# Kernel optimization log

Hardware: AMD Instinct MI355X
Metric: run time of the kernel (lower is better)

Reference implementation:

```python
import jax, jax.numpy as jnp
import numpy as np

B, H, S, DK = 2, 16, 2048, 64


def setup_inputs() -> dict:
    key = jax.random.key(0)
    kq, kk, kv = jax.random.split(key, 3)
    q = jax.random.normal(kq, (B, H, S, DK), dtype=jnp.float32)
    k = jax.random.normal(kk, (B, H, S, DK), dtype=jnp.float32)
    v = jax.random.normal(kv, (B, H, S, DK), dtype=jnp.float32)
    # 3-D boolean mask [B, Sq, Sk]; True = allowed. Causal lower-triangular.
    mask = jnp.broadcast_to(jnp.tril(jnp.ones((S, S), dtype=bool)), (B, S, S))
    return {"q": q, "k": k, "v": v, "mask": mask}


def reference(q, k, v, mask):
    # scores: [B, H, Sq, Sk]
    scores = jnp.einsum("bhqd,bhkd->bhqk", q, k) / jnp.sqrt(jnp.asarray(DK, q.dtype))
    if mask.ndim == scores.ndim - 1:
        mask = mask[:, None, :, :]  # broadcast over heads
    scores = jnp.where(mask, scores, jnp.asarray(-jnp.inf, scores.dtype))
    attn = jax.nn.softmax(scores, axis=-1)
    out = jnp.einsum("bhqk,bhkd->bhqd", attn, v)
    return out
```

## Files before the change

kernel.cpp:

```cpp
#include <hip/hip_runtime.h>


typedef float    v4f __attribute__((ext_vector_type(4)));
typedef _Float16 v4h __attribute__((ext_vector_type(4)));
typedef _Float16 v8h __attribute__((ext_vector_type(8)));

#define SEQ 2048
#define DKC 64

#if __has_builtin(__builtin_amdgcn_exp2f)
#define EXP2(x) __builtin_amdgcn_exp2f(x)
#else
#define EXP2(x) exp2f(x)
#endif

#define MFMA16(a,b,c) __builtin_amdgcn_mfma_f32_16x16x32_f16(a,b,c,0,0,0)
#undef MFMA16
#define MFMA16(a,b,c) __builtin_amdgcn_mfma_f32_16x16x16f16(a,b,c,0,0,0)
#define MFMA32(a,b,c) __builtin_amdgcn_mfma_f32_16x16x32_f16(a,b,c,0,0,0)

__global__ __launch_bounds__(256) void prep_k(const float* __restrict__ k,
                                              _Float16* __restrict__ kh) {
  const int bh = blockIdx.x;
  const int kt = blockIdx.y;
  const int tid  = threadIdx.x;
  const int quad = tid & 3;
  const int l16  = (tid >> 2) & 15;
  const int st   = (tid >> 6) & 1;
  const int s    = tid >> 7;
  const int krow = kt * 32 + s * 16 + l16;
  const int d    = st * 32 + quad * 8;
  const float* src = k + ((size_t)bh * SEQ + krow) * DKC + d;
  float4 a = *(const float4*)src;
  float4 b = *(const float4*)(src + 4);
  v8h h;
  h[0] = (_Float16)a.x; h[1] = (_Float16)a.y; h[2] = (_Float16)a.z; h[3] = (_Float16)a.w;
  h[4] = (_Float16)b.x; h[5] = (_Float16)b.y; h[6] = (_Float16)b.z; h[7] = (_Float16)b.w;
  _Float16* dst = kh + (size_t)bh * SEQ * DKC
                     + (size_t)(kt * 4 + s * 2 + st) * 512 + l16 * 32 + quad * 8;
  *(v8h*)dst = h;
}

__global__ __launch_bounds__(256) void tr_v(const float* __restrict__ v,
                                            _Float16* __restrict__ vt) {
  const int bh = blockIdx.x, kc = blockIdx.y;
  const int d  = threadIdx.x & 63, kq = threadIdx.x >> 6;
  const float* src = v + ((size_t)bh * SEQ + kc * 64) * DKC;
  _Float16* dstb = vt + (size_t)bh * SEQ * DKC + (size_t)kc * 64 * DKC;
#pragma unroll
  for (int kbl = 0; kbl < 4; ++kbl) {
    const int kl0 = kbl * 16 + kq * 4;
    float x0 = src[(size_t)(kl0 + 0) * DKC + d];
    float x1 = src[(size_t)(kl0 + 1) * DKC + d];
    float x2 = src[(size_t)(kl0 + 2) * DKC + d];
    float x3 = src[(size_t)(kl0 + 3) * DKC + d];
    v4h h;
    h[0] = (_Float16)x0; h[1] = (_Float16)x1; h[2] = (_Float16)x2; h[3] = (_Float16)x3;
    *(v4h*)(dstb + ((size_t)(kbl * 64 + d)) * 16 + kq * 4) = h;
  }
}

__device__ __forceinline__ void load_chunk(const _Float16* __restrict__ khb,
                                           const _Float16* __restrict__ vtb,
                                           int kt, int kOff, int vOff,
                                           v8h (&kf)[4], v4h (&va)[8]) {
  const _Float16* kp = khb + (size_t)kt * 2048;
  const _Float16* vp = vtb + (size_t)kt * 2048;
#pragma unroll
  for (int i = 0; i < 4; ++i) kf[i] = *(const v8h*)(kp + i * 512 + kOff);
#pragma unroll
  for (int i = 0; i < 8; ++i) va[i] = *(const v4h*)(vp + i * 256 + vOff);
}

__device__ __forceinline__ void compute_chunk(int kt, int wkt, int qw, int l16, int quad,
                                              const v8h (&qf)[2][2],
                                              const v8h (&kf)[4], const v4h (&va)[8],
                                              v4f (&O)[2][4], v4f (&L)[2],
                                              const v4h ones) {
  v4f S[2][2] = {};
#pragma unroll
  for (int t = 0; t < 2; ++t)
#pragma unroll
    for (int s = 0; s < 2; ++s) {
      S[t][s] = MFMA32(kf[s * 2 + 0], qf[t][0], S[t][s]);
      S[t][s] = MFMA32(kf[s * 2 + 1], qf[t][1], S[t][s]);
    }

  if (kt == wkt - 1) {
    const int k0 = kt * 32;
#pragma unroll
    for (int t = 0; t < 2; ++t) {
      const int qg = qw + t * 16 + l16;
#pragma unroll
      for (int s = 0; s < 2; ++s) {
        const int kb = k0 + s * 16 + quad * 4;
#pragma unroll
        for (int r = 0; r < 4; ++r)
          if (kb + r > qg) S[t][s][r] = -3e38f;
      }
    }
  }

  v4h pf[2][2];
#pragma unroll
  for (int t = 0; t < 2; ++t)
#pragma unroll
    for (int s = 0; s < 2; ++s) {
      v4h p;
#pragma unroll
      for (int r = 0; r < 4; ++r) p[r] = (_Float16)EXP2(S[t][s][r]);
      pf[t][s] = p;
    }

#pragma unroll
  for (int dc = 0; dc < 4; ++dc) {
    O[0][dc] = MFMA16(va[0 * 4 + dc], pf[0][0], O[0][dc]);
    O[0][dc] = MFMA16(va[1 * 4 + dc], pf[0][1], O[0][dc]);
    O[1][dc] = MFMA16(va[0 * 4 + dc], pf[1][0], O[1][dc]);
    O[1][dc] = MFMA16(va[1 * 4 + dc], pf[1][1], O[1][dc]);
  }
  L[0] = MFMA16(ones, pf[0][0], L[0]);
  L[0] = MFMA16(ones, pf[0][1], L[0]);
  L[1] = MFMA16(ones, pf[1][0], L[1]);
  L[1] = MFMA16(ones, pf[1][1], L[1]);
}

__global__ __launch_bounds__(128, 2) void fa_fwd(const float* __restrict__ q,
                                                 const _Float16* __restrict__ kh,
                                                 const _Float16* __restrict__ vt,
                                                 float* __restrict__ out) {
  const int lane = threadIdx.x & 63;
  const int wid  = threadIdx.x >> 6;
  const int quad = lane >> 4;
  const int l16  = lane & 15;

  const int bh = blockIdx.x & 31;
  const int pr = (int)blockIdx.x >> 5;
  const int qp = wid ? (63 - pr) : pr;
  const int qw = qp * 32;
  const size_t base = (size_t)bh * SEQ * DKC;
  const _Float16* khb = kh + base;
  const _Float16* vtb = vt + base;

  const float CSC = 0.18033688011112042f;
  v8h qf[2][2];
#pragma unroll
  for (int t = 0; t < 2; ++t)
#pragma unroll
    for (int st = 0; st < 2; ++st) {
      const float* qr = q + base + (size_t)(qw + t * 16 + l16) * DKC + st * 32 + quad * 8;
      float4 a = *(const float4*)qr;
      float4 b = *(const float4*)(qr + 4);
      v8h h;
      h[0] = (_Float16)(a.x * CSC); h[1] = (_Float16)(a.y * CSC);
      h[2] = (_Float16)(a.z * CSC); h[3] = (_Float16)(a.w * CSC);
      h[4] = (_Float16)(b.x * CSC); h[5] = (_Float16)(b.y * CSC);
      h[6] = (_Float16)(b.z * CSC); h[7] = (_Float16)(b.w * CSC);
      qf[t][st] = h;
    }

  v4f O[2][4] = {};
  v4f L[2]    = {};
  const v4h ones = {(_Float16)1.f, (_Float16)1.f, (_Float16)1.f, (_Float16)1.f};

  const int wkt = qp + 1;
  const int kOff = l16 * 32 + quad * 8;
  const int vOff = l16 * 16 + quad * 4;

  v8h kfA[4], kfB[4];
  v4h vaA[8], vaB[8];

  load_chunk(khb, vtb, 0, kOff, vOff, kfA, vaA);

  int kt = 0;
  while (true) {
    if (kt + 1 < wkt) load_chunk(khb, vtb, kt + 1, kOff, vOff, kfB, vaB);
    compute_chunk(kt, wkt, qw, l16, quad, qf, kfA, vaA, O, L, ones);
    if (++kt >= wkt) break;

    if (kt + 1 < wkt) load_chunk(khb, vtb, kt + 1, kOff, vOff, kfA, vaA);
    compute_chunk(kt, wkt, qw, l16, quad, qf, kfB, vaB, O, L, ones);
    if (++kt >= wkt) break;
  }

#pragma unroll
  for (int t = 0; t < 2; ++t) {
    const float inv = 1.0f / L[t][0];
    float* orow = out + base + (size_t)(qw + t * 16 + l16) * DKC + quad * 4;
#pragma unroll
    for (int dc = 0; dc < 4; ++dc) {
      float4 w;
      w.x = O[t][dc][0] * inv; w.y = O[t][dc][1] * inv;
      w.z = O[t][dc][2] * inv; w.w = O[t][dc][3] * inv;
      *(float4*)(orow + dc * 16) = w;
    }
  }
}

extern "C" void kernel_launch(void* const* d_in, const int* in_sizes, int n_in,
                              void* d_out, int out_size, void* d_ws, size_t ws_size,
                              hipStream_t stream) {
  (void)in_sizes; (void)n_in; (void)out_size; (void)ws_size;
  const float* q = (const float*)d_in[0];
  const float* k = (const float*)d_in[1];
  const float* v = (const float*)d_in[2];
  float* out = (float*)d_out;

  _Float16* kh = (_Float16*)d_ws;
  _Float16* vt = (_Float16*)((char*)d_ws + (size_t)32 * SEQ * DKC * 2);

  prep_k<<<dim3(32, 64), dim3(256), 0, stream>>>(k, kh);
  tr_v<<<dim3(32, 32), dim3(256), 0, stream>>>(v, vt);
  fa_fwd<<<dim3(1024), dim3(128), 0, stream>>>(q, kh, vt, out);
}
```

Before: 146.8 us.

## Split each query tile's key range across two waves and merge via LDS

Previously each wave in a block handled one of two paired query tiles (short and long causal rows) over the full key range. Now both waves process the same query tile together, each covering half of its key chunks, and then handle the paired tile. Partial O and L accumulators are merged through shared memory before the output is written. The V transpose layout also changes so each lane loads 8-half vectors instead of 4-half ones, with fewer loads per chunk. This evens out per-wave work and shortens the critical path, at the cost of two block barriers and LDS traffic per tile.

```diff
diff --git a/kernel.cpp b/kernel.cpp
--- a/kernel.cpp
+++ b/kernel.cpp
@@ -14,8 +14,6 @@
 #define EXP2(x) exp2f(x)
 #endif
 
-#define MFMA16(a,b,c) __builtin_amdgcn_mfma_f32_16x16x32_f16(a,b,c,0,0,0)
-#undef MFMA16
 #define MFMA16(a,b,c) __builtin_amdgcn_mfma_f32_16x16x16f16(a,b,c,0,0,0)
 #define MFMA32(a,b,c) __builtin_amdgcn_mfma_f32_16x16x32_f16(a,b,c,0,0,0)
 
@@ -43,40 +41,34 @@
 
 __global__ __launch_bounds__(256) void tr_v(const float* __restrict__ v,
                                             _Float16* __restrict__ vt) {
-  const int bh = blockIdx.x, kc = blockIdx.y;
-  const int d  = threadIdx.x & 63, kq = threadIdx.x >> 6;
-  const float* src = v + ((size_t)bh * SEQ + kc * 64) * DKC;
-  _Float16* dstb = vt + (size_t)bh * SEQ * DKC + (size_t)kc * 64 * DKC;
-#pragma unroll
-  for (int kbl = 0; kbl < 4; ++kbl) {
-    const int kl0 = kbl * 16 + kq * 4;
-    float x0 = src[(size_t)(kl0 + 0) * DKC + d];
-    float x1 = src[(size_t)(kl0 + 1) * DKC + d];
-    float x2 = src[(size_t)(kl0 + 2) * DKC + d];
-    float x3 = src[(size_t)(kl0 + 3) * DKC + d];
-    v4h h;
-    h[0] = (_Float16)x0; h[1] = (_Float16)x1; h[2] = (_Float16)x2; h[3] = (_Float16)x3;
-    *(v4h*)(dstb + ((size_t)(kbl * 64 + d)) * 16 + kq * 4) = h;
-  }
-}
-
-__device__ __forceinline__ void load_chunk(const _Float16* __restrict__ khb,
-                                           const _Float16* __restrict__ vtb,
-                                           int kt, int kOff, int vOff,
-                                           v8h (&kf)[4], v4h (&va)[8]) {
-  const _Float16* kp = khb + (size_t)kt * 2048;
-  const _Float16* vp = vtb + (size_t)kt * 2048;
-#pragma unroll
-  for (int i = 0; i < 4; ++i) kf[i] = *(const v8h*)(kp + i * 512 + kOff);
-#pragma unroll
-  for (int i = 0; i < 8; ++i) va[i] = *(const v4h*)(vp + i * 256 + vOff);
+  const int bh = blockIdx.x, kt = blockIdx.y;
+  const int d = threadIdx.x & 63, quad = threadIdx.x >> 6;
+  const float* src = v + ((size_t)bh * SEQ + kt * 32) * DKC + d;
+  v8h h;
+#pragma unroll
+  for (int j = 0; j < 4; ++j) h[j]     = (_Float16)src[(size_t)(quad * 4 + j) * DKC];
+#pragma unroll
+  for (int j = 0; j < 4; ++j) h[4 + j] = (_Float16)src[(size_t)(16 + quad * 4 + j) * DKC];
+  _Float16* dst = vt + (size_t)bh * SEQ * DKC + (size_t)kt * 2048
+                     + (d >> 4) * 512 + (quad * 16 + (d & 15)) * 8;
+  *(v8h*)dst = h;
+}
+
+__device__ __forceinline__ void load_chunk(const _Float16* __restrict__ khl,
+                                           const _Float16* __restrict__ vtl,
+                                           int kt, v8h (&kf)[4], v8h (&va)[4]) {
+  const _Float16* kp = khl + (size_t)kt * 2048;
+  const _Float16* vp = vtl + (size_t)kt * 2048;
+#pragma unroll
+  for (int i = 0; i < 4; ++i) kf[i] = *(const v8h*)(kp + i * 512);
+#pragma unroll
+  for (int i = 0; i < 4; ++i) va[i] = *(const v8h*)(vp + i * 512);
 }
 
 __device__ __forceinline__ void compute_chunk(int kt, int wkt, int qw, int l16, int quad,
                                               const v8h (&qf)[2][2],
-                                              const v8h (&kf)[4], const v4h (&va)[8],
-                                              v4f (&O)[2][4], v4f (&L)[2],
-                                              const v4h ones) {
+                                              const v8h (&kf)[4], const v8h (&va)[4],
+                                              v4f (&O)[2][4], v4f (&L)[2], const v4h ones) {
   v4f S[2][2] = {};
 #pragma unroll
   for (int t = 0; t < 2; ++t)
@@ -114,10 +106,12 @@
 
 #pragma unroll
   for (int dc = 0; dc < 4; ++dc) {
-    O[0][dc] = MFMA16(va[0 * 4 + dc], pf[0][0], O[0][dc]);
-    O[0][dc] = MFMA16(va[1 * 4 + dc], pf[0][1], O[0][dc]);
-    O[1][dc] = MFMA16(va[0 * 4 + dc], pf[1][0], O[1][dc]);
-    O[1][dc] = MFMA16(va[1 * 4 + dc], pf[1][1], O[1][dc]);
+    v4h lo = __builtin_shufflevector(va[dc], va[dc], 0, 1, 2, 3);
+    v4h hi = __builtin_shufflevector(va[dc], va[dc], 4, 5, 6, 7);
+    O[0][dc] = MFMA16(lo, pf[0][0], O[0][dc]);
+    O[0][dc] = MFMA16(hi, pf[0][1], O[0][dc]);
+    O[1][dc] = MFMA16(lo, pf[1][0], O[1][dc]);
+    O[1][dc] = MFMA16(hi, pf[1][1], O[1][dc]);
   }
   L[0] = MFMA16(ones, pf[0][0], L[0]);
   L[0] = MFMA16(ones, pf[0][1], L[0]);
@@ -129,6 +123,8 @@
                                                  const _Float16* __restrict__ kh,
                                                  const _Float16* __restrict__ vt,
                                                  float* __restrict__ out) {
+  __shared__ v4f lbuf[10][64];
+
   const int lane = threadIdx.x & 63;
   const int wid  = threadIdx.x >> 6;
   const int quad = lane >> 4;
@@ -136,63 +132,84 @@
 
   const int bh = blockIdx.x & 31;
   const int pr = (int)blockIdx.x >> 5;
-  const int qp = wid ? (63 - pr) : pr;
-  const int qw = qp * 32;
   const size_t base = (size_t)bh * SEQ * DKC;
-  const _Float16* khb = kh + base;
-  const _Float16* vtb = vt + base;
+  const _Float16* khl = kh + base + l16 * 32 + quad * 8;
+  const _Float16* vtl = vt + base + (quad * 16 + l16) * 8;
 
   const float CSC = 0.18033688011112042f;
-  v8h qf[2][2];
-#pragma unroll
-  for (int t = 0; t < 2; ++t)
-#pragma unroll
-    for (int st = 0; st < 2; ++st) {
-      const float* qr = q + base + (size_t)(qw + t * 16 + l16) * DKC + st * 32 + quad * 8;
-      float4 a = *(const float4*)qr;
-      float4 b = *(const float4*)(qr + 4);
-      v8h h;
-      h[0] = (_Float16)(a.x * CSC); h[1] = (_Float16)(a.y * CSC);
-      h[2] = (_Float16)(a.z * CSC); h[3] = (_Float16)(a.w * CSC);
-      h[4] = (_Float16)(b.x * CSC); h[5] = (_Float16)(b.y * CSC);
-      h[6] = (_Float16)(b.z * CSC); h[7] = (_Float16)(b.w * CSC);
-      qf[t][st] = h;
-    }
-
-  v4f O[2][4] = {};
-  v4f L[2]    = {};
   const v4h ones = {(_Float16)1.f, (_Float16)1.f, (_Float16)1.f, (_Float16)1.f};
 
-  const int wkt = qp + 1;
-  const int kOff = l16 * 32 + quad * 8;
-  const int vOff = l16 * 16 + quad * 4;
-
-  v8h kfA[4], kfB[4];
-  v4h vaA[8], vaB[8];
-
-  load_chunk(khb, vtb, 0, kOff, vOff, kfA, vaA);
-
-  int kt = 0;
-  while (true) {
-    if (kt + 1 < wkt) load_chunk(khb, vtb, kt + 1, kOff, vOff, kfB, vaB);
-    compute_chunk(kt, wkt, qw, l16, quad, qf, kfA, vaA, O, L, ones);
-    if (++kt >= wkt) break;
-
-    if (kt + 1 < wkt) load_chunk(khb, vtb, kt + 1, kOff, vOff, kfA, vaA);
-    compute_chunk(kt, wkt, qw, l16, quad, qf, kfB, vaB, O, L, ones);
-    if (++kt >= wkt) break;
-  }
-
-#pragma unroll
-  for (int t = 0; t < 2; ++t) {
-    const float inv = 1.0f / L[t][0];
-    float* orow = out + base + (size_t)(qw + t * 16 + l16) * DKC + quad * 4;
-#pragma unroll
-    for (int dc = 0; dc < 4; ++dc) {
-      float4 w;
-      w.x = O[t][dc][0] * inv; w.y = O[t][dc][1] * inv;
-      w.z = O[t][dc][2] * inv; w.w = O[t][dc][3] * inv;
-      *(float4*)(orow + dc * 16) = w;
+#pragma unroll
+  for (int ph = 0; ph < 2; ++ph) {
+    const int qp  = ph ? (63 - pr) : pr;
+    const int qw  = qp * 32;
+    const int wkt = qp + 1;
+    const int h   = (wkt + 1) >> 1;
+    const int kb  = wid ? h : 0;
+    const int ke  = wid ? wkt : h;
+
+    v8h qf[2][2];
+#pragma unroll
+    for (int t = 0; t < 2; ++t)
+#pragma unroll
+      for (int st = 0; st < 2; ++st) {
+        const float* qr = q + base + (size_t)(qw + t * 16 + l16) * DKC + st * 32 + quad * 8;
+        float4 a = *(const float4*)qr;
+        float4 b = *(const float4*)(qr + 4);
+        v8h hq;
+        hq[0] = (_Float16)(a.x * CSC); hq[1] = (_Float16)(a.y * CSC);
+        hq[2] = (_Float16)(a.z * CSC); hq[3] = (_Float16)(a.w * CSC);
+        hq[4] = (_Float16)(b.x * CSC); hq[5] = (_Float16)(b.y * CSC);
+        hq[6] = (_Float16)(b.z * CSC); hq[7] = (_Float16)(b.w * CSC);
+        qf[t][st] = hq;
+      }
+
+    v4f O[2][4] = {};
+    v4f L[2]    = {};
+
+    if (kb < ke) {
+      v8h kfA[4], kfB[4], vaA[4], vaB[4];
+      load_chunk(khl, vtl, kb, kfA, vaA);
+      int kt = kb;
+      while (true) {
+        if (kt + 1 < ke) load_chunk(khl, vtl, kt + 1, kfB, vaB);
+        compute_chunk(kt, wkt, qw, l16, quad, qf, kfA, vaA, O, L, ones);
+        if (++kt >= ke) break;
+        if (kt + 1 < ke) load_chunk(khl, vtl, kt + 1, kfA, vaA);
+        compute_chunk(kt, wkt, qw, l16, quad, qf, kfB, vaB, O, L, ones);
+        if (++kt >= ke) break;
+      }
+    }
+
+    __syncthreads();
+    if (wid == 0) {
+#pragma unroll
+      for (int t = 0; t < 2; ++t) {
+#pragma unroll
+        for (int dc = 0; dc < 4; ++dc) lbuf[t * 4 + dc][lane] = O[t][dc];
+        lbuf[8 + t][lane] = L[t];
+      }
+    }
+    __syncthreads();
+    if (wid == 1) {
+#pragma unroll
+      for (int t = 0; t < 2; ++t) {
+#pragma unroll
+        for (int dc = 0; dc < 4; ++dc) O[t][dc] += lbuf[t * 4 + dc][lane];
+        L[t] += lbuf[8 + t][lane];
+      }
+#pragma unroll
+      for (int t = 0; t < 2; ++t) {
+        const float inv = 1.0f / L[t][0];
+        float* orow = out + base + (size_t)(qw + t * 16 + l16) * DKC + quad * 4;
+#pragma unroll
+        for (int dc = 0; dc < 4; ++dc) {
+          float4 w;
+          w.x = O[t][dc][0] * inv; w.y = O[t][dc][1] * inv;
+          w.z = O[t][dc][2] * inv; w.w = O[t][dc][3] * inv;
+          *(float4*)(orow + dc * 16) = w;
+        }
+      }
     }
   }
 }
@@ -210,6 +227,6 @@
   _Float16* vt = (_Float16*)((char*)d_ws + (size_t)32 * SEQ * DKC * 2);
 
   prep_k<<<dim3(32, 64), dim3(256), 0, stream>>>(k, kh);
-  tr_v<<<dim3(32, 32), dim3(256), 0, stream>>>(v, vt);
+  tr_v<<<dim3(32, 64), dim3(256), 0, stream>>>(v, vt);
   fa_fwd<<<dim3(1024), dim3(128), 0, stream>>>(q, kh, vt, out);
 }
```

Result: faster. 135.6 us (-7.6%).
